# Optimization experiments

Hardware: AMD Instinct MI355X
Metric: run time of the kernel (lower is better)

Reference implementation:

```python
import jax, jax.numpy as jnp
import numpy as np

EPS = 1e-12   # F.normalize default eps
TH = 0.5      # forward-arg default threshold
CLAMP_LO, CLAMP_HI = 0.01, 0.999


def setup_inputs() -> dict:
    key = jax.random.key(0)
    k1, k2 = jax.random.split(key)
    # x4: ResNet layer3 features after ala1 scaling + upfeat, stride-16 of a 1024px image
    x4 = jax.random.normal(k1, (8, 1024, 64, 64), dtype=jnp.float32)
    # logits: classifier output after upfeat, same spatial grid, 21 classes
    logits = jax.random.normal(k2, (8, 21, 64, 64), dtype=jnp.float32)
    return {"x4": x4, "logits": logits, "pcm": 2}


def reference(x4, logits, pcm):
    b, c, h, w = x4.shape
    hw = h * w
    xf = x4.reshape(b, c, hw)                      # [b, c, hw]
    # F.normalize(dim=1): x / max(||x||_2, eps)
    norm = jnp.sqrt(jnp.sum(xf * xf, axis=1, keepdims=True))
    xn = xf / jnp.maximum(norm, EPS)
    # pixel affinity: [b, hw, hw]
    aff = jnp.einsum('bci,bcj->bij', xn, xn)
    aff = jnp.clip(aff, CLAMP_LO, CLAMP_HI)
    aff = jnp.where(aff < TH, jnp.zeros((), aff.dtype), aff)
    # column-normalize (torch sum over dim=1)
    aff = aff / jnp.sum(aff, axis=1, keepdims=True)
    lf = logits.reshape(b, -1, hw)                 # [b, K, hw]
    for _ in range(pcm):                           # pcm is a Python int
        lf = jnp.einsum('bki,bij->bkj', lf, aff)
    return lf.reshape(b, -1, h, w)
```

## Files before the change

kernel.cpp:

```cpp
#include <hip/hip_runtime.h>
#include <hip/hip_bf16.h>

#define B_  8
#define C_  1024
#define HW_ 4096
#define NK  21
#define NT  32
#define NTRI (NT * (NT + 1) / 2)

using bf16 = __hip_bfloat16;
typedef __attribute__((ext_vector_type(4))) float float4_;
typedef __attribute__((ext_vector_type(8))) int int8v;

__global__ __launch_bounds__(256) void ktrans(const float* __restrict__ x4, float* __restrict__ sumsq,
                                              unsigned char* __restrict__ Xq) {
    int b = blockIdx.z, ct = blockIdx.y, jt = blockIdx.x;
    int c0 = ct * 128, j0 = jt * 64;
    int t = threadIdx.x;
    __shared__ float tile[128][65];
    __shared__ float ssq[64];

    int jl = t & 63, cl = t >> 6;
    if (t < 64) ssq[t] = 0.f;
    __syncthreads();
    float part = 0.f;
#pragma unroll
    for (int cc = 0; cc < 128; cc += 4) {
        float v = x4[((size_t)b * C_ + c0 + cc + cl) * HW_ + j0 + jl];
        tile[cc + cl][jl] = v;
        part = fmaf(v, v, part);
    }
    atomicAdd(&ssq[jl], part);
    __syncthreads();

    int j = t >> 2, q = t & 3;
    int jg = j0 + j;
    unsigned int pk[8];
#pragma unroll
    for (int g = 0; g < 8; ++g) {
        float f0 = tile[q * 32 + g * 4 + 0][j];
        float f1 = tile[q * 32 + g * 4 + 1][j];
        float f2 = tile[q * 32 + g * 4 + 2][j];
        float f3 = tile[q * 32 + g * 4 + 3][j];
        unsigned int r = 0;
        r = __builtin_amdgcn_cvt_pk_fp8_f32(f0, f1, r, false);
        r = __builtin_amdgcn_cvt_pk_fp8_f32(f2, f3, r, true);
        pk[g] = r;
    }
    unsigned char* dst = Xq + ((size_t)b * HW_ + jg) * C_ + c0 + q * 32;
    *(uint4*)(dst)      = make_uint4(pk[0], pk[1], pk[2], pk[3]);
    *(uint4*)(dst + 16) = make_uint4(pk[4], pk[5], pk[6], pk[7]);

    if (t < 64) atomicAdd(&sumsq[b * HW_ + j0 + t], ssq[t]);
}

__global__ __launch_bounds__(256) void kgram(const unsigned char* __restrict__ Xq,
                                             const float* __restrict__ sumsq, bf16* __restrict__ aff,
                                             float* __restrict__ colsum, int* __restrict__ flags) {
    int b = blockIdx.y;
    int p = blockIdx.x;
    int it = (int)((2.0f * NT + 1.0f - sqrtf((2.0f * NT + 1.0f) * (2.0f * NT + 1.0f) - 8.0f * (float)p)) * 0.5f);
    while (it > 0 && p < it * NT - it * (it - 1) / 2) --it;
    while (p >= (it + 1) * NT - (it + 1) * it / 2) ++it;
    int jt = it + p - (it * NT - it * (it - 1) / 2);

    int i0 = it * 128, j0 = jt * 128;
    int t = threadIdx.x, w = t >> 6, l = t & 63;
    int wr = w >> 1, wc = w & 1;
    int lrow = l & 15, lk = l >> 4;

    __shared__ __align__(16) unsigned char As[128 * 128];
    __shared__ __align__(16) unsigned char Bs[128 * 128];
    __shared__ int fl;

    const unsigned char* XA = Xq + ((size_t)b * HW_ + i0) * C_;
    const unsigned char* XB = Xq + ((size_t)b * HW_ + j0) * C_;

    int srow = l >> 3;
    int sslot = l & 7;

    float4_ acc[4][4];
#pragma unroll
    for (int m = 0; m < 4; ++m)
#pragma unroll
        for (int n = 0; n < 4; ++n) acc[m][n] = {0.f, 0.f, 0.f, 0.f};

    for (int k0 = 0; k0 < C_; k0 += 128) {
        __syncthreads();
#pragma unroll
        for (int q = 0; q < 4; ++q) {
            int R = (w * 4 + q) * 8 + srow;
            int gp = sslot ^ (R & 7);
            __builtin_amdgcn_global_load_lds(
                (const __attribute__((address_space(1))) void*)(XA + (size_t)R * C_ + k0 + gp * 16),
                (__attribute__((address_space(3))) void*)(As + R * 128 + sslot * 16), 16, 0, 0);
            __builtin_amdgcn_global_load_lds(
                (const __attribute__((address_space(1))) void*)(XB + (size_t)R * C_ + k0 + gp * 16),
                (__attribute__((address_space(3))) void*)(Bs + R * 128 + sslot * 16), 16, 0, 0);
        }
        __syncthreads();

        int8v av[4], bv[4];
#pragma unroll
        for (int m = 0; m < 4; ++m) {
            int r = wr * 64 + m * 16 + lrow;
            uint4 lo = *(const uint4*)(As + r * 128 + (((lk * 2) ^ (r & 7)) * 16));
            uint4 hi = *(const uint4*)(As + r * 128 + (((lk * 2 + 1) ^ (r & 7)) * 16));
            int8v v; v[0] = lo.x; v[1] = lo.y; v[2] = lo.z; v[3] = lo.w;
            v[4] = hi.x; v[5] = hi.y; v[6] = hi.z; v[7] = hi.w;
            av[m] = v;
        }
#pragma unroll
        for (int n = 0; n < 4; ++n) {
            int r = wc * 64 + n * 16 + lrow;
            uint4 lo = *(const uint4*)(Bs + r * 128 + (((lk * 2) ^ (r & 7)) * 16));
            uint4 hi = *(const uint4*)(Bs + r * 128 + (((lk * 2 + 1) ^ (r & 7)) * 16));
            int8v v; v[0] = lo.x; v[1] = lo.y; v[2] = lo.z; v[3] = lo.w;
            v[4] = hi.x; v[5] = hi.y; v[6] = hi.z; v[7] = hi.w;
            bv[n] = v;
        }
#pragma unroll
        for (int m = 0; m < 4; ++m)
#pragma unroll
            for (int n = 0; n < 4; ++n)
                acc[m][n] = __builtin_amdgcn_mfma_scale_f32_16x16x128_f8f6f4(
                    av[m], bv[n], acc[m][n], 0, 0, 0, 0x7f7f7f7f, 0, 0x7f7f7f7f);
    }

    float rnj[4], rni[4][4];
#pragma unroll
    for (int n = 0; n < 4; ++n) {
        int j = j0 + wc * 64 + n * 16 + lrow;
        rnj[n] = 1.0f / fmaxf(sqrtf(sumsq[b * HW_ + j]), 1e-12f);
    }
#pragma unroll
    for (int m = 0; m < 4; ++m)
#pragma unroll
        for (int r = 0; r < 4; ++r) {
            int i = i0 + wr * 64 + m * 16 + lk * 4 + r;
            rni[m][r] = 1.0f / fmaxf(sqrtf(sumsq[b * HW_ + i]), 1e-12f);
        }
#pragma unroll
    for (int m = 0; m < 4; ++m)
#pragma unroll
        for (int n = 0; n < 4; ++n)
#pragma unroll
            for (int r = 0; r < 4; ++r)
                acc[m][n][r] *= rni[m][r] * rnj[n];

    bool any = false;
#pragma unroll
    for (int m = 0; m < 4; ++m)
#pragma unroll
        for (int n = 0; n < 4; ++n)
#pragma unroll
            for (int r = 0; r < 4; ++r) any |= (acc[m][n][r] >= 0.5f);

    if (t == 0) fl = 0;
    __syncthreads();
    unsigned long long bal = __ballot(any);
    if (l == 0 && bal != 0ull) atomicOr(&fl, 1);
    __syncthreads();
    bool mirror = (it != jt);
    if (t == 0) {
        flags[(b * NT + it) * NT + jt] = fl;
        if (mirror) flags[(b * NT + jt) * NT + it] = fl;
    }

    if (fl) {
        size_t affb = (size_t)b * HW_ * HW_;
        float rsum[4][4];
#pragma unroll
        for (int m = 0; m < 4; ++m)
#pragma unroll
            for (int r = 0; r < 4; ++r) rsum[m][r] = 0.f;

#pragma unroll
        for (int n = 0; n < 4; ++n) {
            int j = j0 + wc * 64 + n * 16 + lrow;
            float cs = 0.f;
#pragma unroll
            for (int m = 0; m < 4; ++m) {
#pragma unroll
                for (int r = 0; r < 4; ++r) {
                    float v = acc[m][n][r];
                    v = fminf(fmaxf(v, 0.01f), 0.999f);
                    v = (v < 0.5f) ? 0.0f : v;
                    bf16 bb = __float2bfloat16(v);
                    int i = i0 + wr * 64 + m * 16 + lk * 4 + r;
                    aff[affb + (size_t)i * HW_ + j] = bb;
                    float bf = __bfloat162float(bb);
                    cs += bf;
                    rsum[m][r] += bf;
                    if (mirror) aff[affb + (size_t)j * HW_ + i] = bb;
                }
            }
            cs += __shfl_xor(cs, 16);
            cs += __shfl_xor(cs, 32);
            if (lk == 0) atomicAdd(&colsum[b * HW_ + j], cs);
        }
        if (mirror) {
#pragma unroll
            for (int m = 0; m < 4; ++m) {
#pragma unroll
                for (int r = 0; r < 4; ++r) {
                    float s = rsum[m][r];
                    s += __shfl_xor(s, 1);
                    s += __shfl_xor(s, 2);
                    s += __shfl_xor(s, 4);
                    s += __shfl_xor(s, 8);
                    if (lrow == 0) {
                        int i = i0 + wr * 64 + m * 16 + lk * 4 + r;
                        atomicAdd(&colsum[b * HW_ + i], s);
                    }
                }
            }
        }
    }
}

__global__ __launch_bounds__(128) void kprop(const float* __restrict__ lf, const bf16* __restrict__ aff,
                                             const int* __restrict__ flags, const float* __restrict__ colsum,
                                             float* __restrict__ outp) {
    int b = blockIdx.y, jt = blockIdx.x;
    int t = threadIdx.x;
    int j = jt * 128 + t;
    __shared__ float lfs[NK * 128];
    float acc[NK];
#pragma unroll
    for (int k = 0; k < NK; ++k) acc[k] = 0.f;

    for (int it = 0; it < NT; ++it) {
        if (flags[(b * NT + it) * NT + jt] == 0) continue;
        __syncthreads();
        for (int idx = t; idx < NK * 128; idx += 128)
            lfs[idx] = lf[((size_t)b * NK + (idx >> 7)) * HW_ + it * 128 + (idx & 127)];
        __syncthreads();
        const bf16* ap = aff + ((size_t)b * HW_ + it * 128) * HW_ + j;
        for (int ii = 0; ii < 128; ++ii) {
            float a = __bfloat162float(ap[(size_t)ii * HW_]);
#pragma unroll
            for (int k = 0; k < NK; ++k)
                acc[k] = fmaf(lfs[(k << 7) + ii], a, acc[k]);
        }
    }
    float inv = 1.0f / colsum[b * HW_ + j];
#pragma unroll
    for (int k = 0; k < NK; ++k)
        outp[((size_t)b * NK + k) * HW_ + j] = acc[k] * inv;
}

extern "C" void kernel_launch(void* const* d_in, const int* in_sizes, int n_in,
                              void* d_out, int out_size, void* d_ws, size_t ws_size,
                              hipStream_t stream) {
    const float* x4 = (const float*)d_in[0];
    const float* logits = (const float*)d_in[1];
    float* out = (float*)d_out;

    char* w = (char*)d_ws;
    size_t off = 0;
    auto take = [&](size_t bytes) {
        char* p = w + off;
        off += (bytes + 255) & ~(size_t)255;
        return p;
    };
    unsigned char* Xq = (unsigned char*)take((size_t)B_ * HW_ * C_);
    bf16* aff     = (bf16*)take((size_t)B_ * HW_ * HW_ * 2);
    float* colsum = (float*)take((size_t)B_ * HW_ * 4);
    int*   flags  = (int*)take((size_t)B_ * NT * NT * 4);
    float* sumsq  = (float*)take((size_t)B_ * HW_ * 4);
    float* lf1    = (float*)take((size_t)B_ * NK * HW_ * 4);

    hipMemsetAsync(colsum, 0, (size_t)B_ * HW_ * 4 + (size_t)B_ * NT * NT * 4 + (size_t)B_ * HW_ * 4, stream);

    ktrans<<<dim3(HW_ / 64, C_ / 128, B_), dim3(256), 0, stream>>>(x4, sumsq, Xq);
    kgram <<<dim3(NTRI, B_), dim3(256), 0, stream>>>(Xq, sumsq, aff, colsum, flags);

    kprop<<<dim3(NT, B_), dim3(128), 0, stream>>>(logits, aff, flags, colsum, lf1);
    kprop<<<dim3(NT, B_), dim3(128), 0, stream>>>(lf1, aff, flags, colsum, out);
}
```

Before: 354.5 us.

## Enlarge gram tiles to 256x256 with double-buffered LDS prefetch pipeline

The fp8 Gram kernel now has each 512-thread block compute a 256x256 tile instead of a 128x128 one. This cuts redundant global loads of the quantized features per output element. K-chunks are staged into a 128KB double-buffered LDS region with explicit vmcnt waits, so loads overlap MFMA work, and s_setprio is raised around the MFMA bursts. Block indices interleave batches, and the sparsity flags become 16x16 per batch. As a result, kprop visits all four 128-row sub-tiles of any flagged 256 block, which can add propagation work. The large LDS footprint also limits occupancy to one block per CU.

```diff
diff --git a/kernel.cpp b/kernel.cpp
--- a/kernel.cpp
+++ b/kernel.cpp
@@ -1,16 +1,21 @@
 #include <hip/hip_runtime.h>
 #include <hip/hip_bf16.h>
 
-#define B_  8
-#define C_  1024
-#define HW_ 4096
-#define NK  21
-#define NT  32
-#define NTRI (NT * (NT + 1) / 2)
+#define B_   8
+#define C_   1024
+#define HW_  4096
+#define NK   21
+#define NT   32
+#define NT2  16
+#define NTRI2 (NT2 * (NT2 + 1) / 2)
 
 using bf16 = __hip_bfloat16;
 typedef __attribute__((ext_vector_type(4))) float float4_;
 typedef __attribute__((ext_vector_type(8))) int int8v;
+
+#define WAITV(n) asm volatile("s_waitcnt vmcnt(" #n ")" ::: "memory")
+#define FENCE()  asm volatile("" ::: "memory")
+#define BARRIER() do { FENCE(); __builtin_amdgcn_s_barrier(); FENCE(); } while (0)
 
 __global__ __launch_bounds__(256) void ktrans(const float* __restrict__ x4, float* __restrict__ sumsq,
                                               unsigned char* __restrict__ Xq) {
@@ -54,124 +59,148 @@
     if (t < 64) atomicAdd(&sumsq[b * HW_ + j0 + t], ssq[t]);
 }
 
-__global__ __launch_bounds__(256) void kgram(const unsigned char* __restrict__ Xq,
-                                             const float* __restrict__ sumsq, bf16* __restrict__ aff,
-                                             float* __restrict__ colsum, int* __restrict__ flags) {
-    int b = blockIdx.y;
-    int p = blockIdx.x;
-    int it = (int)((2.0f * NT + 1.0f - sqrtf((2.0f * NT + 1.0f) * (2.0f * NT + 1.0f) - 8.0f * (float)p)) * 0.5f);
-    while (it > 0 && p < it * NT - it * (it - 1) / 2) --it;
-    while (p >= (it + 1) * NT - (it + 1) * it / 2) ++it;
-    int jt = it + p - (it * NT - it * (it - 1) / 2);
-
-    int i0 = it * 128, j0 = jt * 128;
-    int t = threadIdx.x, w = t >> 6, l = t & 63;
-    int wr = w >> 1, wc = w & 1;
+__global__ __launch_bounds__(512, 2) void kgram(const unsigned char* __restrict__ Xq,
+                                                const float* __restrict__ sumsq, bf16* __restrict__ aff,
+                                                float* __restrict__ colsum, int* __restrict__ flags) {
+    int lin = blockIdx.x;
+    int b = lin & 7;
+    int p = lin >> 3;
+    int it = (int)((2.0f * NT2 + 1.0f - sqrtf((2.0f * NT2 + 1.0f) * (2.0f * NT2 + 1.0f) - 8.0f * (float)p)) * 0.5f);
+    while (it > 0 && p < it * NT2 - it * (it - 1) / 2) --it;
+    while (p >= (it + 1) * NT2 - (it + 1) * it / 2) ++it;
+    int jt = it + p - (it * NT2 - it * (it - 1) / 2);
+
+    int i0 = it * 256, j0 = jt * 256;
+    int tid = threadIdx.x, w = tid >> 6, l = tid & 63;
+    int wr = w >> 2, wc = w & 3;
     int lrow = l & 15, lk = l >> 4;
 
-    __shared__ __align__(16) unsigned char As[128 * 128];
-    __shared__ __align__(16) unsigned char Bs[128 * 128];
+    __shared__ __align__(16) unsigned char smem[131072];
     __shared__ int fl;
 
     const unsigned char* XA = Xq + ((size_t)b * HW_ + i0) * C_;
     const unsigned char* XB = Xq + ((size_t)b * HW_ + j0) * C_;
 
-    int srow = l >> 3;
-    int sslot = l & 7;
-
-    float4_ acc[4][4];
-#pragma unroll
-    for (int m = 0; m < 4; ++m)
+    int rhi = tid >> 3, sl = tid & 7, gp = sl ^ (rhi & 7);
+
+    auto stg = [&](int bo, const unsigned char* g, int k0) {
+#pragma unroll
+        for (int q = 0; q < 4; ++q) {
+            int R = q * 64 + rhi;
+            __builtin_amdgcn_global_load_lds(
+                (const __attribute__((address_space(1))) void*)(g + (size_t)R * C_ + k0 + (gp << 4)),
+                (__attribute__((address_space(3))) void*)(smem + bo + R * 128 + (sl << 4)), 16, 0, 0);
+        }
+    };
+
+    auto ldfrag = [&](const unsigned char* base, int r) {
+        int sw = r & 7;
+        uint4 lo = *(const uint4*)(base + r * 128 + (((lk * 2) ^ sw) << 4));
+        uint4 hi = *(const uint4*)(base + r * 128 + (((lk * 2 + 1) ^ sw) << 4));
+        int8v v; v[0] = lo.x; v[1] = lo.y; v[2] = lo.z; v[3] = lo.w;
+        v[4] = hi.x; v[5] = hi.y; v[6] = hi.z; v[7] = hi.w;
+        return v;
+    };
+
+    float4_ acc[8][4];
+#pragma unroll
+    for (int m = 0; m < 8; ++m)
 #pragma unroll
         for (int n = 0; n < 4; ++n) acc[m][n] = {0.f, 0.f, 0.f, 0.f};
 
-    for (int k0 = 0; k0 < C_; k0 += 128) {
-        __syncthreads();
-#pragma unroll
-        for (int q = 0; q < 4; ++q) {
-            int R = (w * 4 + q) * 8 + srow;
-            int gp = sslot ^ (R & 7);
-            __builtin_amdgcn_global_load_lds(
-                (const __attribute__((address_space(1))) void*)(XA + (size_t)R * C_ + k0 + gp * 16),
-                (__attribute__((address_space(3))) void*)(As + R * 128 + sslot * 16), 16, 0, 0);
-            __builtin_amdgcn_global_load_lds(
-                (const __attribute__((address_space(1))) void*)(XB + (size_t)R * C_ + k0 + gp * 16),
-                (__attribute__((address_space(3))) void*)(Bs + R * 128 + sslot * 16), 16, 0, 0);
-        }
-        __syncthreads();
-
-        int8v av[4], bv[4];
-#pragma unroll
-        for (int m = 0; m < 4; ++m) {
-            int r = wr * 64 + m * 16 + lrow;
-            uint4 lo = *(const uint4*)(As + r * 128 + (((lk * 2) ^ (r & 7)) * 16));
-            uint4 hi = *(const uint4*)(As + r * 128 + (((lk * 2 + 1) ^ (r & 7)) * 16));
-            int8v v; v[0] = lo.x; v[1] = lo.y; v[2] = lo.z; v[3] = lo.w;
-            v[4] = hi.x; v[5] = hi.y; v[6] = hi.z; v[7] = hi.w;
-            av[m] = v;
-        }
-#pragma unroll
-        for (int n = 0; n < 4; ++n) {
-            int r = wc * 64 + n * 16 + lrow;
-            uint4 lo = *(const uint4*)(Bs + r * 128 + (((lk * 2) ^ (r & 7)) * 16));
-            uint4 hi = *(const uint4*)(Bs + r * 128 + (((lk * 2 + 1) ^ (r & 7)) * 16));
-            int8v v; v[0] = lo.x; v[1] = lo.y; v[2] = lo.z; v[3] = lo.w;
-            v[4] = hi.x; v[5] = hi.y; v[6] = hi.z; v[7] = hi.w;
-            bv[n] = v;
-        }
+    auto ck = [&](int bo) {
+        const unsigned char* A  = smem + bo;
+        const unsigned char* Bb = smem + bo + 32768;
+        int8v bv[4];
+#pragma unroll
+        for (int n = 0; n < 4; ++n) bv[n] = ldfrag(Bb, wc * 64 + n * 16 + lrow);
+        int8v av[4];
+#pragma unroll
+        for (int m = 0; m < 4; ++m) av[m] = ldfrag(A, wr * 128 + m * 16 + lrow);
+        __builtin_amdgcn_s_setprio(1);
 #pragma unroll
         for (int m = 0; m < 4; ++m)
 #pragma unroll
             for (int n = 0; n < 4; ++n)
                 acc[m][n] = __builtin_amdgcn_mfma_scale_f32_16x16x128_f8f6f4(
                     av[m], bv[n], acc[m][n], 0, 0, 0, 0x7f7f7f7f, 0, 0x7f7f7f7f);
-    }
-
-    float rnj[4], rni[4][4];
+        __builtin_amdgcn_s_setprio(0);
+#pragma unroll
+        for (int m = 0; m < 4; ++m) av[m] = ldfrag(A, wr * 128 + (m + 4) * 16 + lrow);
+        __builtin_amdgcn_s_setprio(1);
+#pragma unroll
+        for (int m = 0; m < 4; ++m)
+#pragma unroll
+            for (int n = 0; n < 4; ++n)
+                acc[m + 4][n] = __builtin_amdgcn_mfma_scale_f32_16x16x128_f8f6f4(
+                    av[m], bv[n], acc[m + 4][n], 0, 0, 0, 0x7f7f7f7f, 0, 0x7f7f7f7f);
+        __builtin_amdgcn_s_setprio(0);
+    };
+
+    stg(0, XA, 0);        stg(32768, XB, 0);
+    stg(65536, XA, 128);  stg(98304, XB, 128);
+
+    for (int tt2 = 0; tt2 < 3; ++tt2) {
+        int kb = tt2 * 256;
+        WAITV(8);
+        BARRIER();
+        ck(0);
+        BARRIER();
+        stg(0, XA, kb + 256); stg(32768, XB, kb + 256);
+        WAITV(8);
+        BARRIER();
+        ck(65536);
+        BARRIER();
+        stg(65536, XA, kb + 384); stg(98304, XB, kb + 384);
+    }
+    WAITV(8);
+    BARRIER();
+    ck(0);
+    WAITV(0);
+    BARRIER();
+    ck(65536);
+
+    float rnj[4];
 #pragma unroll
     for (int n = 0; n < 4; ++n) {
         int j = j0 + wc * 64 + n * 16 + lrow;
         rnj[n] = 1.0f / fmaxf(sqrtf(sumsq[b * HW_ + j]), 1e-12f);
     }
-#pragma unroll
-    for (int m = 0; m < 4; ++m)
+    float rni[8][4];
+#pragma unroll
+    for (int m = 0; m < 8; ++m)
 #pragma unroll
         for (int r = 0; r < 4; ++r) {
-            int i = i0 + wr * 64 + m * 16 + lk * 4 + r;
+            int i = i0 + wr * 128 + m * 16 + lk * 4 + r;
             rni[m][r] = 1.0f / fmaxf(sqrtf(sumsq[b * HW_ + i]), 1e-12f);
         }
-#pragma unroll
-    for (int m = 0; m < 4; ++m)
+    bool any = false;
+#pragma unroll
+    for (int m = 0; m < 8; ++m)
 #pragma unroll
         for (int n = 0; n < 4; ++n)
 #pragma unroll
-            for (int r = 0; r < 4; ++r)
+            for (int r = 0; r < 4; ++r) {
                 acc[m][n][r] *= rni[m][r] * rnj[n];
-
-    bool any = false;
-#pragma unroll
-    for (int m = 0; m < 4; ++m)
-#pragma unroll
-        for (int n = 0; n < 4; ++n)
-#pragma unroll
-            for (int r = 0; r < 4; ++r) any |= (acc[m][n][r] >= 0.5f);
-
-    if (t == 0) fl = 0;
+                any |= (acc[m][n][r] >= 0.5f);
+            }
+
+    if (tid == 0) fl = 0;
     __syncthreads();
     unsigned long long bal = __ballot(any);
     if (l == 0 && bal != 0ull) atomicOr(&fl, 1);
     __syncthreads();
     bool mirror = (it != jt);
-    if (t == 0) {
-        flags[(b * NT + it) * NT + jt] = fl;
-        if (mirror) flags[(b * NT + jt) * NT + it] = fl;
+    if (tid == 0) {
+        flags[(b * NT2 + it) * NT2 + jt] = fl;
+        if (mirror) flags[(b * NT2 + jt) * NT2 + it] = fl;
     }
 
     if (fl) {
         size_t affb = (size_t)b * HW_ * HW_;
-        float rsum[4][4];
-#pragma unroll
-        for (int m = 0; m < 4; ++m)
+        float rsum[8][4];
+#pragma unroll
+        for (int m = 0; m < 8; ++m)
 #pragma unroll
             for (int r = 0; r < 4; ++r) rsum[m][r] = 0.f;
 
@@ -180,14 +209,14 @@
             int j = j0 + wc * 64 + n * 16 + lrow;
             float cs = 0.f;
 #pragma unroll
-            for (int m = 0; m < 4; ++m) {
+            for (int m = 0; m < 8; ++m) {
 #pragma unroll
                 for (int r = 0; r < 4; ++r) {
                     float v = acc[m][n][r];
                     v = fminf(fmaxf(v, 0.01f), 0.999f);
                     v = (v < 0.5f) ? 0.0f : v;
                     bf16 bb = __float2bfloat16(v);
-                    int i = i0 + wr * 64 + m * 16 + lk * 4 + r;
+                    int i = i0 + wr * 128 + m * 16 + lk * 4 + r;
                     aff[affb + (size_t)i * HW_ + j] = bb;
                     float bf = __bfloat162float(bb);
                     cs += bf;
@@ -201,7 +230,7 @@
         }
         if (mirror) {
 #pragma unroll
-            for (int m = 0; m < 4; ++m) {
+            for (int m = 0; m < 8; ++m) {
 #pragma unroll
                 for (int r = 0; r < 4; ++r) {
                     float s = rsum[m][r];
@@ -210,7 +239,7 @@
                     s += __shfl_xor(s, 4);
                     s += __shfl_xor(s, 8);
                     if (lrow == 0) {
-                        int i = i0 + wr * 64 + m * 16 + lk * 4 + r;
+                        int i = i0 + wr * 128 + m * 16 + lk * 4 + r;
                         atomicAdd(&colsum[b * HW_ + i], s);
                     }
                 }
@@ -231,7 +260,7 @@
     for (int k = 0; k < NK; ++k) acc[k] = 0.f;
 
     for (int it = 0; it < NT; ++it) {
-        if (flags[(b * NT + it) * NT + jt] == 0) continue;
+        if (flags[(b * NT2 + (it >> 1)) * NT2 + (jt >> 1)] == 0) continue;
         __syncthreads();
         for (int idx = t; idx < NK * 128; idx += 128)
             lfs[idx] = lf[((size_t)b * NK + (idx >> 7)) * HW_ + it * 128 + (idx & 127)];
@@ -267,14 +296,15 @@
     unsigned char* Xq = (unsigned char*)take((size_t)B_ * HW_ * C_);
     bf16* aff     = (bf16*)take((size_t)B_ * HW_ * HW_ * 2);
     float* colsum = (float*)take((size_t)B_ * HW_ * 4);
-    int*   flags  = (int*)take((size_t)B_ * NT * NT * 4);
+    int*   flags  = (int*)take((size_t)B_ * NT2 * NT2 * 4);
     float* sumsq  = (float*)take((size_t)B_ * HW_ * 4);
     float* lf1    = (float*)take((size_t)B_ * NK * HW_ * 4);
 
-    hipMemsetAsync(colsum, 0, (size_t)B_ * HW_ * 4 + (size_t)B_ * NT * NT * 4 + (size_t)B_ * HW_ * 4, stream);
+    hipMemsetAsync(colsum, 0,
+                   (size_t)B_ * HW_ * 4 + (size_t)B_ * NT2 * NT2 * 4 + (size_t)B_ * HW_ * 4, stream);
 
     ktrans<<<dim3(HW_ / 64, C_ / 128, B_), dim3(256), 0, stream>>>(x4, sumsq, Xq);
-    kgram <<<dim3(NTRI, B_), dim3(256), 0, stream>>>(Xq, sumsq, aff, colsum, flags);
+    kgram <<<dim3(NTRI2 * B_), dim3(512), 0, stream>>>(Xq, sumsq, aff, colsum, flags);
 
     kprop<<<dim3(NT, B_), dim3(128), 0, stream>>>(logits, aff, flags, colsum, lf1);
     kprop<<<dim3(NT, B_), dim3(128), 0, stream>>>(lf1, aff, flags, colsum, out);
```

Measured after the change: 441.8 us. 24.6% more time.
